# Optimization experiments

Hardware: AMD Instinct MI355X
Metric: run time of the kernel (lower is better)

Reference implementation:

```python
import jax, jax.numpy as jnp
import numpy as np
from jax import lax

B, H, W, C = 16, 56, 56, 256
NH = 8
KD = C // NH  # key/head dim = 32
FF = 1024
EPS = 1e-6
SCALE = KD ** -0.5


def _layernorm(x, g, b):
    m = jnp.mean(x, axis=-1, keepdims=True)
    v = jnp.mean(jnp.square(x - m), axis=-1, keepdims=True)
    return (x - m) * lax.rsqrt(v + EPS) * g + b


def _dwconv(x, w, b):
    # x: (B,H,W,Cd), w: (kh,kw,1,Cd) depthwise (groups = Cd), stride 1, SAME padding
    return lax.conv_general_dilated(
        x, w, window_strides=(1, 1), padding='SAME',
        dimension_numbers=('NHWC', 'HWIO', 'NHWC'),
        feature_group_count=x.shape[-1]) + b


def setup_inputs() -> dict:
    key = jax.random.key(0)
    ks = jax.random.split(key, 20)
    r = lambda i, shape, s=0.02: jax.random.normal(ks[i], shape, jnp.float32) * s
    return {
        'x': jax.random.normal(ks[0], (B, H, W, C), jnp.float32),
        'mask_h': jax.random.normal(ks[1], (NH, H, H), jnp.float32),
        'mask_w': jax.random.normal(ks[2], (NH, W, W), jnp.float32),
        # pos: DWConv2d(C, 3, 1, 1)
        'pos_w': r(3, (3, 3, 1, C)), 'pos_b': jnp.zeros((C,), jnp.float32),
        # retention layer norm
        'ln1_g': jnp.ones((C,), jnp.float32), 'ln1_b': jnp.zeros((C,), jnp.float32),
        # MaSA projections (stored as (in, out) so y = x @ W + b)
        'q_w': r(4, (C, C)), 'q_b': jnp.zeros((C,), jnp.float32),
        'k_w': r(5, (C, C)), 'k_b': jnp.zeros((C,), jnp.float32),
        'v_w': r(6, (C, C)), 'v_b': jnp.zeros((C,), jnp.float32),
        # lepe: DWConv2d(C, 5, 1, 2)
        'lepe_w': r(7, (5, 5, 1, C)), 'lepe_b': jnp.zeros((C,), jnp.float32),
        'out_w': r(8, (C, C)), 'out_b': jnp.zeros((C,), jnp.float32),
        # final layer norm
        'ln2_g': jnp.ones((C,), jnp.float32), 'ln2_b': jnp.zeros((C,), jnp.float32),
        # FFN
        'fc1_w': r(9, (C, FF)), 'fc1_b': jnp.zeros((FF,), jnp.float32),
        'fc2_w': r(10, (FF, C)), 'fc2_b': jnp.zeros((C,), jnp.float32),
    }


def _masa(x, mask_h, mask_w, q_w, q_b, k_w, k_b, v_w, v_b, lepe_w, lepe_b, out_w, out_b):
    b, h, w, _ = x.shape
    q = x @ q_w + q_b
    k = (x @ k_w + k_b) * SCALE
    v = x @ v_w + v_b
    lepe = _dwconv(v, lepe_w, lepe_b)
    qh = q.reshape(b, h, w, NH, KD)
    kh = k.reshape(b, h, w, NH, KD)
    vh = v.reshape(b, h, w, NH, KD)
    # width-axis retention: scores (b, h, NH, w, w), mask_w broadcasts as (NH, w, w)
    attn_w = jax.nn.softmax(jnp.einsum('bhqnd,bhknd->bhnqk', qh, kh) + mask_w, axis=-1)
    vw = jnp.einsum('bhnqk,bhknd->bhnqd', attn_w, vh)  # (b, h, NH, w, KD)
    # height-axis retention: scores (b, w, NH, h, h), mask_h broadcasts as (NH, h, h)
    attn_h = jax.nn.softmax(jnp.einsum('bqwnd,bkwnd->bwnqk', qh, kh) + mask_h, axis=-1)
    out = jnp.einsum('bwnqk,bknwd->bqwnd', attn_h, vw)  # (b, h, w, NH, KD)
    out = out.reshape(b, h, w, NH * KD) + lepe
    return out @ out_w + out_b


def reference(x, mask_h, mask_w, pos_w, pos_b, ln1_g, ln1_b,
              q_w, q_b, k_w, k_b, v_w, v_b, lepe_w, lepe_b, out_w, out_b,
              ln2_g, ln2_b, fc1_w, fc1_b, fc2_w, fc2_b):
    # RetBlock (retention='whole', no layerscale, no dropout / drop_path)
    x = x + _dwconv(x, pos_w, pos_b)
    x = x + _masa(_layernorm(x, ln1_g, ln1_b), mask_h, mask_w,
                  q_w, q_b, k_w, k_b, v_w, v_b, lepe_w, lepe_b, out_w, out_b)
    y = _layernorm(x, ln2_g, ln2_b)
    y = jax.nn.gelu(y @ fc1_w + fc1_b, approximate=False) @ fc2_w + fc2_b
    return x + y
```

## Files before the change

### kernel.cpp

```cpp
#include <hip/hip_runtime.h>
#include <hip/hip_bf16.h>
#include <math.h>
#include <stdint.h>

typedef __bf16 bf16;
typedef __bf16 bf16x8 __attribute__((ext_vector_type(8)));
typedef __bf16 bf16x4 __attribute__((ext_vector_type(4)));
typedef float f32x4 __attribute__((ext_vector_type(4)));

#define NPIX (16*56*56)
#define CH 256
#define SCALE_K 0.17677669529663687f

__global__ void wt_kernel(const float* __restrict__ w, float scale, int K, int N,
                          bf16* __restrict__ out)
{
    int total = K * N;
    for (int idx = blockIdx.x * blockDim.x + threadIdx.x; idx < total;
         idx += gridDim.x * blockDim.x) {
        int n = idx / K, k = idx - n * K;
        out[idx] = (bf16)(w[(size_t)k * N + n] * scale);
    }
}

__global__ void qkv_bias_kernel(const float* __restrict__ qb,
                                const float* __restrict__ kb,
                                const float* __restrict__ vb,
                                float* __restrict__ out)
{
    int i = blockIdx.x * blockDim.x + threadIdx.x;
    if (i < 256) out[i] = qb[i];
    else if (i < 512) out[i] = kb[i - 256] * SCALE_K;
    else if (i < 768) out[i] = vb[i - 512];
}

__global__ __launch_bounds__(256) void posconv_ln_kernel(
    const float* __restrict__ x, const float* __restrict__ w,
    const float* __restrict__ bias, const float* __restrict__ g,
    const float* __restrict__ bta, float* __restrict__ x1,
    bf16* __restrict__ tln)
{
    const int wave = threadIdx.x >> 6, lane = threadIdx.x & 63;
    const long pix = (long)blockIdx.x * 4 + wave;
    const int ww = (int)(pix % 56);
    const int hh = (int)((pix / 56) % 56);
    const int b  = (int)(pix / 3136);
    const int c  = lane * 4;
    float4 acc = ((const float4*)(bias + c))[0];
    float4 xin = ((const float4*)(x + pix * 256 + c))[0];
    acc.x += xin.x; acc.y += xin.y; acc.z += xin.z; acc.w += xin.w;
    #pragma unroll
    for (int dh = 0; dh < 3; ++dh) {
        int h2 = hh + dh - 1;
        if (h2 < 0 || h2 >= 56) continue;
        #pragma unroll
        for (int dw = 0; dw < 3; ++dw) {
            int w2 = ww + dw - 1;
            if (w2 < 0 || w2 >= 56) continue;
            float4 xv = ((const float4*)(x + (((long)(b * 56 + h2)) * 56 + w2) * 256 + c))[0];
            float4 wv = ((const float4*)(w + (dh * 3 + dw) * 256 + c))[0];
            acc.x += xv.x * wv.x; acc.y += xv.y * wv.y;
            acc.z += xv.z * wv.z; acc.w += xv.w * wv.w;
        }
    }
    ((float4*)(x1 + pix * 256 + c))[0] = acc;
    float s  = acc.x + acc.y + acc.z + acc.w;
    float q2 = acc.x * acc.x + acc.y * acc.y + acc.z * acc.z + acc.w * acc.w;
    #pragma unroll
    for (int o = 32; o; o >>= 1) {
        s  += __shfl_xor(s,  o, 64);
        q2 += __shfl_xor(q2, o, 64);
    }
    float mean = s * (1.0f / 256.0f);
    float var  = q2 * (1.0f / 256.0f) - mean * mean;
    float rs   = rsqrtf(var + 1e-6f);
    float4 gv = ((const float4*)g)[lane];
    float4 bv = ((const float4*)bta)[lane];
    bf16* o4 = tln + pix * 256 + c;
    o4[0] = (bf16)((acc.x - mean) * rs * gv.x + bv.x);
    o4[1] = (bf16)((acc.y - mean) * rs * gv.y + bv.y);
    o4[2] = (bf16)((acc.z - mean) * rs * gv.z + bv.z);
    o4[3] = (bf16)((acc.w - mean) * rs * gv.w + bv.w);
}

__global__ __launch_bounds__(256) void lepe_kernel(
    const bf16* __restrict__ qkv, const float* __restrict__ w,
    const float* __restrict__ bias, bf16* __restrict__ out)
{
    long idx = (long)blockIdx.x * 256 + threadIdx.x;
    int c8 = (int)(idx & 31);
    long pix = idx >> 5;
    int ww = (int)(pix % 56);
    int hh = (int)((pix / 56) % 56);
    int b  = (int)(pix / 3136);
    int c  = c8 * 8;
    float acc[8];
    #pragma unroll
    for (int j = 0; j < 8; ++j) acc[j] = bias[c + j];
    #pragma unroll
    for (int dh = 0; dh < 5; ++dh) {
        int h2 = hh + dh - 2;
        if (h2 < 0 || h2 >= 56) continue;
        #pragma unroll
        for (int dw = 0; dw < 5; ++dw) {
            int w2 = ww + dw - 2;
            if (w2 < 0 || w2 >= 56) continue;
            bf16x8 vv = *(const bf16x8*)(qkv + (((long)(b * 56 + h2)) * 56 + w2) * 768 + 512 + c);
            const float4* wp = (const float4*)(w + (dh * 5 + dw) * 256 + c);
            float4 w0 = wp[0], w1 = wp[1];
            acc[0] += (float)vv[0] * w0.x; acc[1] += (float)vv[1] * w0.y;
            acc[2] += (float)vv[2] * w0.z; acc[3] += (float)vv[3] * w0.w;
            acc[4] += (float)vv[4] * w1.x; acc[5] += (float)vv[5] * w1.y;
            acc[6] += (float)vv[6] * w1.z; acc[7] += (float)vv[7] * w1.w;
        }
    }
    bf16* o = out + pix * 256 + c;
    #pragma unroll
    for (int j = 0; j < 8; ++j) o[j] = (bf16)acc[j];
}

__global__ __launch_bounds__(256) void ln_kernel(
    const float* __restrict__ x, const float* __restrict__ g,
    const float* __restrict__ bta, bf16* __restrict__ out)
{
    int wid = threadIdx.x >> 6, lane = threadIdx.x & 63;
    long pix = (long)blockIdx.x * 4 + wid;
    if (pix >= NPIX) return;
    const float4* xr = (const float4*)(x + pix * 256);
    float4 v = xr[lane];
    float s  = v.x + v.y + v.z + v.w;
    float q2 = v.x * v.x + v.y * v.y + v.z * v.z + v.w * v.w;
    #pragma unroll
    for (int o = 32; o; o >>= 1) {
        s  += __shfl_xor(s,  o, 64);
        q2 += __shfl_xor(q2, o, 64);
    }
    float mean = s * (1.0f / 256.0f);
    float var  = q2 * (1.0f / 256.0f) - mean * mean;
    float rs   = rsqrtf(var + 1e-6f);
    float4 gv = ((const float4*)g)[lane];
    float4 bv = ((const float4*)bta)[lane];
    bf16* o4 = out + pix * 256 + lane * 4;
    o4[0] = (bf16)((v.x - mean) * rs * gv.x + bv.x);
    o4[1] = (bf16)((v.y - mean) * rs * gv.y + bv.y);
    o4[2] = (bf16)((v.z - mean) * rs * gv.z + bv.z);
    o4[3] = (bf16)((v.w - mean) * rs * gv.w + bv.w);
}

template<bool WIDTH>
__global__ __launch_bounds__(256) void attn_mfma_kernel(
    const bf16* __restrict__ qkv, const bf16* __restrict__ vsrc,
    const float* __restrict__ mask, const bf16* __restrict__ lepe,
    bf16* __restrict__ outp)
{
    __shared__ bf16 VtAll[4][32][72];
    __shared__ bf16 PlAll[4][16][72];
    const int tid = threadIdx.x;
    const int wave = tid >> 6, lane = tid & 63;
    const int g = lane >> 4, ql = lane & 15;
    const int n  = blockIdx.x / 224;
    const int s  = (blockIdx.x % 224) * 4 + wave;
    const int b  = s / 56, rc = s % 56;
    bf16 (*Vt)[72] = VtAll[wave];
    bf16 (*Pl)[72] = PlAll[wave];
    const long basePix = WIDTH ? ((long)(b * 56 + rc)) * 56 : (long)b * 3136 + rc;
    const long pixStride = WIDTH ? 1 : 56;
    const bf16* qb = qkv + basePix * 768 + n * 32;
    const long qstride = pixStride * 768;
    const bf16* vbp; long vstride;
    if (WIDTH) { vbp = qb + 512; vstride = qstride; }
    else       { vbp = vsrc + basePix * 256 + n * 32; vstride = pixStride * 256; }

    #pragma unroll
    for (int it = 0; it < 2; ++it) {
        int idx = it * 64 + lane;
        if (idx < 112) {
            int pp = idx >> 2, chunk = idx & 3;
            int pos0 = pp * 2;
            bf16x8 v0 = *(const bf16x8*)(vbp + (long)pos0 * vstride + chunk * 8);
            bf16x8 v1 = *(const bf16x8*)(vbp + (long)(pos0 + 1) * vstride + chunk * 8);
            int colb = pos0 ^ (chunk << 3);
            #pragma unroll
            for (int j = 0; j < 8; ++j) {
                union { bf16 h[2]; unsigned int u; } pk;
                pk.h[0] = v0[j]; pk.h[1] = v1[j];
                *(unsigned int*)&Vt[chunk * 8 + j][colb] = pk.u;
            }
        }
    }
    if (lane < 32) {
        int d = lane;
        int colb = 56 ^ ((d >> 3) << 3);
        *(float4*)&Vt[d][colb] = (float4){0.f, 0.f, 0.f, 0.f};
    }

    bf16x8 qf[4], kf[4];
    #pragma unroll
    for (int t4 = 0; t4 < 4; ++t4) {
        int row = ql + 16 * t4; if (row > 55) row = 55;
        qf[t4] = *(const bf16x8*)(qb + (long)row * qstride + 8 * g);
        kf[t4] = *(const bf16x8*)(qb + (long)row * qstride + 256 + 8 * g);
    }

    f32x4 sA[4][4];
    #pragma unroll
    for (int qt = 0; qt < 4; ++qt)
        #pragma unroll
        for (int kt = 0; kt < 4; ++kt)
            sA[qt][kt] = __builtin_amdgcn_mfma_f32_16x16x32_bf16(
                kf[kt], qf[qt], (f32x4){0.f, 0.f, 0.f, 0.f}, 0, 0, 0);

    const float* mrow = mask + n * 3136;
    #pragma unroll
    for (int qt = 0; qt < 4; ++qt) {
        int qm = ql + 16 * qt; if (qm > 55) qm = 55;
        #pragma unroll
        for (int kt = 0; kt < 4; ++kt) {
            if (kt == 3 && g >= 2) {
                sA[qt][3][0] = -3.0e38f; sA[qt][3][1] = -3.0e38f;
                sA[qt][3][2] = -3.0e38f; sA[qt][3][3] = -3.0e38f;
            } else {
                float4 mv = *(const float4*)(mrow + qm * 56 + kt * 16 + 4 * g);
                sA[qt][kt][0] += mv.x; sA[qt][kt][1] += mv.y;
                sA[qt][kt][2] += mv.z; sA[qt][kt][3] += mv.w;
            }
        }
    }

    #pragma unroll
    for (int qt = 0; qt < 4; ++qt) {
        float m = -3.0e38f;
        #pragma unroll
        for (int kt = 0; kt < 4; ++kt)
            #pragma unroll
            for (int r = 0; r < 4; ++r) m = fmaxf(m, sA[qt][kt][r]);
        m = fmaxf(m, __shfl_xor(m, 16, 64));
        m = fmaxf(m, __shfl_xor(m, 32, 64));
        float p[4][4];
        float sum = 0.f;
        #pragma unroll
        for (int kt = 0; kt < 4; ++kt)
            #pragma unroll
            for (int r = 0; r < 4; ++r) {
                float e = exp2f((sA[qt][kt][r] - m) * 1.4426950408889634f);
                p[kt][r] = e; sum += e;
            }
        sum += __shfl_xor(sum, 16, 64);
        sum += __shfl_xor(sum, 32, 64);
        float rinv = 1.0f / sum;
        #pragma unroll
        for (int kt = 0; kt < 4; ++kt) {
            bf16x4 w;
            #pragma unroll
            for (int r = 0; r < 4; ++r) w[r] = (bf16)(p[kt][r] * rinv);
            *(bf16x4*)&Pl[ql][kt * 16 + 4 * g] = w;
        }
        #pragma unroll
        for (int nt = 0; nt < 2; ++nt) {
            f32x4 o = {0.f, 0.f, 0.f, 0.f};
            #pragma unroll
            for (int ks = 0; ks < 2; ++ks) {
                bf16x8 af = *(const bf16x8*)&Pl[ql][ks * 32 + 8 * g];
                int vrow = ql + 16 * nt;
                int vcol = (ks * 32 + 8 * g) ^ ((vrow >> 3) << 3);
                bf16x8 bv = *(const bf16x8*)&Vt[vrow][vcol];
                o = __builtin_amdgcn_mfma_f32_16x16x32_bf16(af, bv, o, 0, 0, 0);
            }
            if (!(qt == 3 && g >= 2)) {
                #pragma unroll
                for (int r = 0; r < 4; ++r) {
                    int q = 16 * qt + 4 * g + r;
                    long addr = (basePix + (long)q * pixStride) * 256 + n * 32 + nt * 16 + ql;
                    float vv = o[r];
                    if (!WIDTH) vv += (float)lepe[addr];
                    outp[addr] = (bf16)vv;
                }
            }
        }
    }
}

template<bool GELU, bool RESID, bool OUT_BF16>
__global__ __launch_bounds__(256) void gemm_kernel(
    const bf16* __restrict__ A, const bf16* __restrict__ Wt,
    const float* __restrict__ bias, const float* __restrict__ resid,
    void* __restrict__ Cout, int M, int N, int K)
{
    __shared__ bf16 As[128 * 64];
    __shared__ bf16 Bs[128 * 64];
    const int t = threadIdx.x;
    const int wave = t >> 6, lane = t & 63;
    const int nTilesN = N >> 7;
    const int q8 = gridDim.x >> 3;
    const int o = ((int)blockIdx.x & 7) * q8 + ((int)blockIdx.x >> 3);
    const int tm = o / nTilesN, tn = o % nTilesN;
    const long m0 = (long)tm * 128, n0 = (long)tn * 128;
    const int waveM = (wave >> 1) * 64, waveN = (wave & 1) * 64;
    f32x4 acc[4][4] = {};

    for (int k0 = 0; k0 < K; k0 += 64) {
        #pragma unroll
        for (int i = 0; i < 4; ++i) {
            int c = i * 256 + wave * 64 + lane;
            int r = c >> 3, cc = (c & 7) * 8;
            const bf16* ga = A  + (m0 + r) * (long)K + k0 + cc;
            const bf16* gb = Wt + (n0 + r) * (long)K + k0 + cc;
            __builtin_amdgcn_global_load_lds(
                (const __attribute__((address_space(1))) void*)ga,
                (__attribute__((address_space(3))) void*)(As + (i * 256 + wave * 64) * 8),
                16, 0, 0);
            __builtin_amdgcn_global_load_lds(
                (const __attribute__((address_space(1))) void*)gb,
                (__attribute__((address_space(3))) void*)(Bs + (i * 256 + wave * 64) * 8),
                16, 0, 0);
        }
        __syncthreads();
        #pragma unroll
        for (int kk = 0; kk < 2; ++kk) {
            bf16x8 af[4], bfr[4];
            const int krow = kk * 32 + (lane >> 4) * 8;
            #pragma unroll
            for (int fm = 0; fm < 4; ++fm)
                af[fm] = *(const bf16x8*)&As[(waveM + fm * 16 + (lane & 15)) * 64 + krow];
            #pragma unroll
            for (int fn = 0; fn < 4; ++fn)
                bfr[fn] = *(const bf16x8*)&Bs[(waveN + fn * 16 + (lane & 15)) * 64 + krow];
            #pragma unroll
            for (int fm = 0; fm < 4; ++fm)
                #pragma unroll
                for (int fn = 0; fn < 4; ++fn)
                    acc[fm][fn] = __builtin_amdgcn_mfma_f32_16x16x32_bf16(
                        af[fm], bfr[fn], acc[fm][fn], 0, 0, 0);
        }
        __syncthreads();
    }

    #pragma unroll
    for (int fm = 0; fm < 4; ++fm) {
        #pragma unroll
        for (int r = 0; r < 4; ++r) {
            const long m = m0 + waveM + fm * 16 + (lane >> 4) * 4 + r;
            #pragma unroll
            for (int fn = 0; fn < 4; ++fn) {
                const long n = n0 + waveN + fn * 16 + (lane & 15);
                float vv = acc[fm][fn][r] + bias[n];
                if (GELU) {
                    float u = vv * (0.7978845608028654f + 0.0356774081f * vv * vv);
                    float tgh = 1.0f - 2.0f / (__expf(2.0f * u) + 1.0f);
                    vv = 0.5f * vv * (1.0f + tgh);
                }
                if (RESID) vv += resid[m * N + n];
                if (OUT_BF16) ((bf16*)Cout)[m * N + n] = (bf16)vv;
                else          ((float*)Cout)[m * N + n] = vv;
            }
        }
    }
}

extern "C" void kernel_launch(void* const* d_in, const int* in_sizes, int n_in,
                              void* d_out, int out_size, void* d_ws, size_t ws_size,
                              hipStream_t stream)
{
    (void)in_sizes; (void)n_in; (void)out_size; (void)ws_size;
    const float* x      = (const float*)d_in[0];
    const float* mask_h = (const float*)d_in[1];
    const float* mask_w = (const float*)d_in[2];
    const float* pos_w  = (const float*)d_in[3];
    const float* pos_b  = (const float*)d_in[4];
    const float* ln1_g  = (const float*)d_in[5];
    const float* ln1_b  = (const float*)d_in[6];
    const float* q_w    = (const float*)d_in[7];
    const float* q_b    = (const float*)d_in[8];
    const float* k_w    = (const float*)d_in[9];
    const float* k_b    = (const float*)d_in[10];
    const float* v_w    = (const float*)d_in[11];
    const float* v_b    = (const float*)d_in[12];
    const float* lepe_w = (const float*)d_in[13];
    const float* lepe_b = (const float*)d_in[14];
    const float* out_w  = (const float*)d_in[15];
    const float* out_b  = (const float*)d_in[16];
    const float* ln2_g  = (const float*)d_in[17];
    const float* ln2_b  = (const float*)d_in[18];
    const float* fc1_w  = (const float*)d_in[19];
    const float* fc1_b  = (const float*)d_in[20];
    const float* fc2_w  = (const float*)d_in[21];
    const float* fc2_b  = (const float*)d_in[22];

    char* ws = (char*)d_ws;
    size_t off = 0;
    auto alloc = [&](size_t bytes) -> void* {
        void* p = ws + off;
        off += (bytes + 255) & ~(size_t)255;
        return p;
    };
    const int M = NPIX;
    float* x1     = (float*)alloc((size_t)M * 256 * 4);
    bf16*  tln    = (bf16*) alloc((size_t)M * 256 * 2);
    bf16*  qkv    = (bf16*) alloc((size_t)M * 768 * 2);
    bf16*  lepeb  = (bf16*) alloc((size_t)M * 256 * 2);
    bf16*  vwb    = (bf16*) alloc((size_t)M * 256 * 2);
    bf16*  obuf   = (bf16*) alloc((size_t)M * 256 * 2);
    bf16*  wt_qkv = (bf16*) alloc((size_t)768 * 256 * 2);
    bf16*  wt_out = (bf16*) alloc((size_t)256 * 256 * 2);
    bf16*  wt_fc1 = (bf16*) alloc((size_t)1024 * 256 * 2);
    bf16*  wt_fc2 = (bf16*) alloc((size_t)256 * 1024 * 2);
    float* qkvb   = (float*)alloc(768 * 4);
    bf16*  h1     = tln;
    float* outf   = (float*)d_out;

    wt_kernel<<<256, 256, 0, stream>>>(q_w, 1.0f, 256, 256, wt_qkv);
    wt_kernel<<<256, 256, 0, stream>>>(k_w, SCALE_K, 256, 256, wt_qkv + 256 * 256);
    wt_kernel<<<256, 256, 0, stream>>>(v_w, 1.0f, 256, 256, wt_qkv + 512 * 256);
    wt_kernel<<<256, 256, 0, stream>>>(out_w, 1.0f, 256, 256, wt_out);
    wt_kernel<<<1024, 256, 0, stream>>>(fc1_w, 1.0f, 256, 1024, wt_fc1);
    wt_kernel<<<1024, 256, 0, stream>>>(fc2_w, 1.0f, 1024, 256, wt_fc2);
    qkv_bias_kernel<<<3, 256, 0, stream>>>(q_b, k_b, v_b, qkvb);

    posconv_ln_kernel<<<12544, 256, 0, stream>>>(x, pos_w, pos_b, ln1_g, ln1_b, x1, tln);
    gemm_kernel<false, false, true><<<392 * 6, 256, 0, stream>>>(
        tln, wt_qkv, qkvb, nullptr, qkv, M, 768, 256);
    lepe_kernel<<<6272, 256, 0, stream>>>(qkv, lepe_w, lepe_b, lepeb);
    attn_mfma_kernel<true><<<1792, 256, 0, stream>>>(qkv, nullptr, mask_w, nullptr, vwb);
    attn_mfma_kernel<false><<<1792, 256, 0, stream>>>(qkv, vwb, mask_h, lepeb, obuf);
    gemm_kernel<false, true, false><<<392 * 2, 256, 0, stream>>>(
        obuf, wt_out, out_b, x1, outf, M, 256, 256);
    ln_kernel<<<12544, 256, 0, stream>>>(outf, ln2_g, ln2_b, lepeb);
    gemm_kernel<true, false, true><<<392 * 8, 256, 0, stream>>>(
        lepeb, wt_fc1, fc1_b, nullptr, h1, M, 1024, 256);
    gemm_kernel<false, true, false><<<392 * 2, 256, 0, stream>>>(
        h1, wt_fc2, fc2_b, outf, outf, M, 256, 1024);
}
```

Before: 444.8 us.

## Fuse out-projection GEMM with residual and LayerNorm; stage bf16 GEMM epilogue through LDS

Replaces the out-projection GEMM plus separate LayerNorm kernel with one kernel in which each block computes a full 128x256 row tile, adds bias and residual, reduces row statistics with lane shuffles, and writes both the fp32 residual stream and the normalized bf16 activations. This removes a full fp32 re-read of the intermediate and one launch. Separately, the bf16-output GEMM epilogue now writes results into shared memory and then stores coalesced 16-byte rows, instead of scattered 2-byte stores. The fused kernel launches only 392 blocks, each holding 128 accumulator registers per thread, so occupancy drops and the grid may underfill the GPU.

Result: no change. 449.0 us (+0.9%).

```diff
diff --git a/kernel.cpp b/kernel.cpp
--- a/kernel.cpp
+++ b/kernel.cpp
@@ -117,34 +117,6 @@
     bf16* o = out + pix * 256 + c;
     #pragma unroll
     for (int j = 0; j < 8; ++j) o[j] = (bf16)acc[j];
-}
-
-__global__ __launch_bounds__(256) void ln_kernel(
-    const float* __restrict__ x, const float* __restrict__ g,
-    const float* __restrict__ bta, bf16* __restrict__ out)
-{
-    int wid = threadIdx.x >> 6, lane = threadIdx.x & 63;
-    long pix = (long)blockIdx.x * 4 + wid;
-    if (pix >= NPIX) return;
-    const float4* xr = (const float4*)(x + pix * 256);
-    float4 v = xr[lane];
-    float s  = v.x + v.y + v.z + v.w;
-    float q2 = v.x * v.x + v.y * v.y + v.z * v.z + v.w * v.w;
-    #pragma unroll
-    for (int o = 32; o; o >>= 1) {
-        s  += __shfl_xor(s,  o, 64);
-        q2 += __shfl_xor(q2, o, 64);
-    }
-    float mean = s * (1.0f / 256.0f);
-    float var  = q2 * (1.0f / 256.0f) - mean * mean;
-    float rs   = rsqrtf(var + 1e-6f);
-    float4 gv = ((const float4*)g)[lane];
-    float4 bv = ((const float4*)bta)[lane];
-    bf16* o4 = out + pix * 256 + lane * 4;
-    o4[0] = (bf16)((v.x - mean) * rs * gv.x + bv.x);
-    o4[1] = (bf16)((v.y - mean) * rs * gv.y + bv.y);
-    o4[2] = (bf16)((v.z - mean) * rs * gv.z + bv.z);
-    o4[3] = (bf16)((v.w - mean) * rs * gv.w + bv.w);
 }
 
 template<bool WIDTH>
@@ -286,8 +258,9 @@
     const float* __restrict__ bias, const float* __restrict__ resid,
     void* __restrict__ Cout, int M, int N, int K)
 {
-    __shared__ bf16 As[128 * 64];
-    __shared__ bf16 Bs[128 * 64];
+    __shared__ bf16 smem[17408];
+    bf16* As = smem;
+    bf16* Bs = smem + 8192;
     const int t = threadIdx.x;
     const int wave = t >> 6, lane = t & 63;
     const int nTilesN = N >> 7;
@@ -335,23 +308,149 @@
         __syncthreads();
     }
 
-    #pragma unroll
-    for (int fm = 0; fm < 4; ++fm) {
+    if constexpr (OUT_BF16) {
+        #pragma unroll
+        for (int fm = 0; fm < 4; ++fm) {
+            #pragma unroll
+            for (int r = 0; r < 4; ++r) {
+                const int mrow = waveM + fm * 16 + (lane >> 4) * 4 + r;
+                #pragma unroll
+                for (int fn = 0; fn < 4; ++fn) {
+                    const int ncol = waveN + fn * 16 + (lane & 15);
+                    float vv = acc[fm][fn][r] + bias[n0 + ncol];
+                    if (GELU) {
+                        float u = vv * (0.7978845608028654f + 0.0356774081f * vv * vv);
+                        float tgh = 1.0f - 2.0f / (__expf(2.0f * u) + 1.0f);
+                        vv = 0.5f * vv * (1.0f + tgh);
+                    }
+                    smem[mrow * 136 + ncol] = (bf16)vv;
+                }
+            }
+        }
+        __syncthreads();
+        const int rrow = t >> 4, rchunk = t & 15;
+        #pragma unroll
+        for (int s = 0; s < 8; ++s) {
+            int row = s * 16 + rrow;
+            bf16x8 val = *(const bf16x8*)&smem[row * 136 + rchunk * 8];
+            *(bf16x8*)((bf16*)Cout + (m0 + row) * (long)N + n0 + rchunk * 8) = val;
+        }
+    } else {
+        #pragma unroll
+        for (int fm = 0; fm < 4; ++fm) {
+            #pragma unroll
+            for (int r = 0; r < 4; ++r) {
+                const long m = m0 + waveM + fm * 16 + (lane >> 4) * 4 + r;
+                #pragma unroll
+                for (int fn = 0; fn < 4; ++fn) {
+                    const long n = n0 + waveN + fn * 16 + (lane & 15);
+                    float vv = acc[fm][fn][r] + bias[n];
+                    if (RESID) vv += resid[m * N + n];
+                    ((float*)Cout)[m * N + n] = vv;
+                }
+            }
+        }
+    }
+}
+
+__global__ __launch_bounds__(256) void outln_kernel(
+    const bf16* __restrict__ A, const bf16* __restrict__ Wt,
+    const float* __restrict__ bias, const float* __restrict__ resid,
+    const float* __restrict__ g2, const float* __restrict__ b2,
+    float* __restrict__ x2out, bf16* __restrict__ uout)
+{
+    __shared__ bf16 As[128 * 64];
+    __shared__ bf16 Bs[256 * 64];
+    const int t = threadIdx.x;
+    const int wave = t >> 6, lane = t & 63;
+    const int g = lane >> 4, ql = lane & 15;
+    const int q8 = gridDim.x >> 3;
+    const int o = ((int)blockIdx.x & 7) * q8 + ((int)blockIdx.x >> 3);
+    const long m0 = (long)o * 128;
+    const int waveM = wave * 32;
+    f32x4 acc[2][16] = {};
+
+    for (int k0 = 0; k0 < 256; k0 += 64) {
+        #pragma unroll
+        for (int i = 0; i < 4; ++i) {
+            int c = i * 256 + wave * 64 + lane;
+            int r = c >> 3, cc = (c & 7) * 8;
+            const bf16* ga = A + (m0 + r) * 256 + k0 + cc;
+            __builtin_amdgcn_global_load_lds(
+                (const __attribute__((address_space(1))) void*)ga,
+                (__attribute__((address_space(3))) void*)(As + (i * 256 + wave * 64) * 8),
+                16, 0, 0);
+        }
+        #pragma unroll
+        for (int i = 0; i < 8; ++i) {
+            int c = i * 256 + wave * 64 + lane;
+            int r = c >> 3, cc = (c & 7) * 8;
+            const bf16* gb = Wt + r * 256 + k0 + cc;
+            __builtin_amdgcn_global_load_lds(
+                (const __attribute__((address_space(1))) void*)gb,
+                (__attribute__((address_space(3))) void*)(Bs + (i * 256 + wave * 64) * 8),
+                16, 0, 0);
+        }
+        __syncthreads();
+        #pragma unroll
+        for (int kk = 0; kk < 2; ++kk) {
+            const int krow = kk * 32 + g * 8;
+            bf16x8 af[2];
+            af[0] = *(const bf16x8*)&As[(waveM + ql) * 64 + krow];
+            af[1] = *(const bf16x8*)&As[(waveM + 16 + ql) * 64 + krow];
+            #pragma unroll
+            for (int fn = 0; fn < 16; ++fn) {
+                bf16x8 bv = *(const bf16x8*)&Bs[(fn * 16 + ql) * 64 + krow];
+                acc[0][fn] = __builtin_amdgcn_mfma_f32_16x16x32_bf16(af[0], bv, acc[0][fn], 0, 0, 0);
+                acc[1][fn] = __builtin_amdgcn_mfma_f32_16x16x32_bf16(af[1], bv, acc[1][fn], 0, 0, 0);
+            }
+        }
+        __syncthreads();
+    }
+
+    float rsum[2][4] = {}, rsq[2][4] = {};
+    #pragma unroll
+    for (int fm = 0; fm < 2; ++fm) {
+        #pragma unroll
+        for (int fn = 0; fn < 16; ++fn) {
+            const int n = fn * 16 + ql;
+            const float bn = bias[n];
+            #pragma unroll
+            for (int r = 0; r < 4; ++r) {
+                const long m = m0 + waveM + fm * 16 + g * 4 + r;
+                float v = acc[fm][fn][r] + bn + resid[m * 256 + n];
+                acc[fm][fn][r] = v;
+                rsum[fm][r] += v; rsq[fm][r] += v * v;
+            }
+        }
+    }
+    #pragma unroll
+    for (int fm = 0; fm < 2; ++fm)
         #pragma unroll
         for (int r = 0; r < 4; ++r) {
-            const long m = m0 + waveM + fm * 16 + (lane >> 4) * 4 + r;
-            #pragma unroll
-            for (int fn = 0; fn < 4; ++fn) {
-                const long n = n0 + waveN + fn * 16 + (lane & 15);
-                float vv = acc[fm][fn][r] + bias[n];
-                if (GELU) {
-                    float u = vv * (0.7978845608028654f + 0.0356774081f * vv * vv);
-                    float tgh = 1.0f - 2.0f / (__expf(2.0f * u) + 1.0f);
-                    vv = 0.5f * vv * (1.0f + tgh);
-                }
-                if (RESID) vv += resid[m * N + n];
-                if (OUT_BF16) ((bf16*)Cout)[m * N + n] = (bf16)vv;
-                else          ((float*)Cout)[m * N + n] = vv;
+            float s = rsum[fm][r], q = rsq[fm][r];
+            #pragma unroll
+            for (int off = 8; off; off >>= 1) {
+                s += __shfl_xor(s, off, 64);
+                q += __shfl_xor(q, off, 64);
+            }
+            float mean = s * (1.0f / 256.0f);
+            float var  = q * (1.0f / 256.0f) - mean * mean;
+            rsum[fm][r] = mean;
+            rsq[fm][r]  = rsqrtf(var + 1e-6f);
+        }
+    #pragma unroll
+    for (int fm = 0; fm < 2; ++fm) {
+        #pragma unroll
+        for (int fn = 0; fn < 16; ++fn) {
+            const int n = fn * 16 + ql;
+            const float gn = g2[n], bn2 = b2[n];
+            #pragma unroll
+            for (int r = 0; r < 4; ++r) {
+                const long m = m0 + waveM + fm * 16 + g * 4 + r;
+                float v = acc[fm][fn][r];
+                x2out[m * 256 + n] = v;
+                uout[m * 256 + n] = (bf16)((v - rsum[fm][r]) * rsq[fm][r] * gn + bn2);
             }
         }
     }
@@ -422,9 +521,8 @@
     lepe_kernel<<<6272, 256, 0, stream>>>(qkv, lepe_w, lepe_b, lepeb);
     attn_mfma_kernel<true><<<1792, 256, 0, stream>>>(qkv, nullptr, mask_w, nullptr, vwb);
     attn_mfma_kernel<false><<<1792, 256, 0, stream>>>(qkv, vwb, mask_h, lepeb, obuf);
-    gemm_kernel<false, true, false><<<392 * 2, 256, 0, stream>>>(
-        obuf, wt_out, out_b, x1, outf, M, 256, 256);
-    ln_kernel<<<12544, 256, 0, stream>>>(outf, ln2_g, ln2_b, lepeb);
+    outln_kernel<<<392, 256, 0, stream>>>(
+        obuf, wt_out, out_b, x1, ln2_g, ln2_b, outf, lepeb);
     gemm_kernel<true, false, true><<<392 * 8, 256, 0, stream>>>(
         lepeb, wt_fc1, fc1_b, nullptr, h1, M, 1024, 256);
     gemm_kernel<false, true, false><<<392 * 2, 256, 0, stream>>>(
```
